# Kernel tuning notes

Hardware: AMD Instinct MI355X
Metric: run time of the kernel (lower is better)

Reference implementation:

```python
import jax, jax.numpy as jnp
import numpy as np

# RecursiveNN: leaves -> embedding lookup; internal node -> sum of two children.
# For a binary tree, the root value equals the sum of all leaf embeddings,
# so the batched faithful form is gather + reduce over the leaf axis.

VOCAB = 100000
DIM = 300
B = 4096   # number of trees (sentences)
L = 64     # leaves per tree


def setup_inputs() -> dict:
    key = jax.random.key(0)
    k1, k2 = jax.random.split(key)
    word_ids = jax.random.randint(k1, (B, L), 0, VOCAB, dtype=jnp.int64 if jax.config.jax_enable_x64 else jnp.int32)
    embedding = jax.random.normal(k2, (VOCAB, DIM), dtype=jnp.float32)
    return {"word_ids": word_ids, "embedding": embedding}


def reference(word_ids, embedding):
    # [B, L, D] gather of leaf embeddings, then child-sum reduction to the root: [B, D]
    leaf_emb = embedding[word_ids]
    return leaf_emb.sum(axis=1)
```

## Files before the change

### kernel.cpp

```cpp
#include <hip/hip_runtime.h>


#define NB 4096
#define NL 64
#define ND 300
#define ND4 75

__global__ __launch_bounds__(256, 4) void recnn_root_sum(
    const int* __restrict__ word_ids,
    const float4* __restrict__ emb4,
    float* __restrict__ out)
{
    __shared__ int ids[NL];
    __shared__ float partial[4][ND];

    const int b    = blockIdx.x;
    const int tid  = threadIdx.x;
    const int wave = tid >> 6;
    const int lane = tid & 63;

    if (tid < NL) ids[tid] = word_ids[b * NL + tid];
    __syncthreads();

    float4 acc0 = make_float4(0.f, 0.f, 0.f, 0.f);
    float4 acc1 = make_float4(0.f, 0.f, 0.f, 0.f);

    const int l0 = wave * 16;
    #pragma unroll
    for (int i = 0; i < 16; ++i) {
        const int row = ids[l0 + i];
        const float4* rp = emb4 + (size_t)row * ND4;
        float4 v0 = rp[lane];
        acc0.x += v0.x; acc0.y += v0.y; acc0.z += v0.z; acc0.w += v0.w;
        if (lane < ND4 - 64) {
            float4 v1 = rp[64 + lane];
            acc1.x += v1.x; acc1.y += v1.y; acc1.z += v1.z; acc1.w += v1.w;
        }
    }

    *reinterpret_cast<float4*>(&partial[wave][lane * 4]) = acc0;
    if (lane < ND4 - 64)
        *reinterpret_cast<float4*>(&partial[wave][256 + lane * 4]) = acc1;
    __syncthreads();

    for (int t = tid; t < ND; t += 256) {
        out[(size_t)b * ND + t] =
            partial[0][t] + partial[1][t] + partial[2][t] + partial[3][t];
    }
}

extern "C" void kernel_launch(void* const* d_in, const int* in_sizes, int n_in,
                              void* d_out, int out_size, void* d_ws, size_t ws_size,
                              hipStream_t stream) {
    const int*    word_ids = (const int*)d_in[0];
    const float4* emb4     = (const float4*)d_in[1];
    float*        out      = (float*)d_out;

    recnn_root_sum<<<NB, 256, 0, stream>>>(word_ids, emb4, out);
}
```

Baseline: 192.3 us.

## Assign one wave per tree and broadcast leaf ids via readlane

Each wave now reduces a whole tree instead of splitting a tree's leaves across four waves. This removes the shared-memory partial sums and both block barriers. Leaf ids are loaded one per lane and broadcast with readlane, and the 11-lane tail runs as a second loop that re-reads the ids. In exchange each wave issues a longer serial chain of 64 dependent-address loads with less parallelism per tree, and the tail loop runs with only 11 lanes active.

```diff
diff --git a/kernel.cpp b/kernel.cpp
--- a/kernel.cpp
+++ b/kernel.cpp
@@ -6,46 +6,39 @@
 #define ND 300
 #define ND4 75
 
-__global__ __launch_bounds__(256, 4) void recnn_root_sum(
+__global__ __launch_bounds__(256, 8) void recnn_root_sum(
     const int* __restrict__ word_ids,
     const float4* __restrict__ emb4,
-    float* __restrict__ out)
+    float4* __restrict__ out4)
 {
-    __shared__ int ids[NL];
-    __shared__ float partial[4][ND];
-
-    const int b    = blockIdx.x;
     const int tid  = threadIdx.x;
     const int wave = tid >> 6;
     const int lane = tid & 63;
+    const int tree = blockIdx.x * 4 + wave;
 
-    if (tid < NL) ids[tid] = word_ids[b * NL + tid];
-    __syncthreads();
+    const int myid = word_ids[tree * NL + lane];
 
     float4 acc0 = make_float4(0.f, 0.f, 0.f, 0.f);
-    float4 acc1 = make_float4(0.f, 0.f, 0.f, 0.f);
 
-    const int l0 = wave * 16;
-    #pragma unroll
-    for (int i = 0; i < 16; ++i) {
-        const int row = ids[l0 + i];
-        const float4* rp = emb4 + (size_t)row * ND4;
-        float4 v0 = rp[lane];
-        acc0.x += v0.x; acc0.y += v0.y; acc0.z += v0.z; acc0.w += v0.w;
-        if (lane < ND4 - 64) {
-            float4 v1 = rp[64 + lane];
-            acc1.x += v1.x; acc1.y += v1.y; acc1.z += v1.z; acc1.w += v1.w;
-        }
+    #pragma unroll 8
+    for (int i = 0; i < NL; ++i) {
+        const int row = __builtin_amdgcn_readlane(myid, i);
+        const float4 v = emb4[(size_t)row * ND4 + lane];
+        acc0.x += v.x; acc0.y += v.y; acc0.z += v.z; acc0.w += v.w;
     }
 
-    *reinterpret_cast<float4*>(&partial[wave][lane * 4]) = acc0;
-    if (lane < ND4 - 64)
-        *reinterpret_cast<float4*>(&partial[wave][256 + lane * 4]) = acc1;
-    __syncthreads();
+    float4* op = out4 + (size_t)tree * ND4;
+    op[lane] = acc0;
 
-    for (int t = tid; t < ND; t += 256) {
-        out[(size_t)b * ND + t] =
-            partial[0][t] + partial[1][t] + partial[2][t] + partial[3][t];
+    if (lane < ND4 - 64) {
+        float4 acc1 = make_float4(0.f, 0.f, 0.f, 0.f);
+        #pragma unroll 8
+        for (int i = 0; i < NL; ++i) {
+            const int row = __builtin_amdgcn_readlane(myid, i);
+            const float4 v = emb4[(size_t)row * ND4 + 64 + lane];
+            acc1.x += v.x; acc1.y += v.y; acc1.z += v.z; acc1.w += v.w;
+        }
+        op[64 + lane] = acc1;
     }
 }
 
@@ -54,7 +47,7 @@
                               hipStream_t stream) {
     const int*    word_ids = (const int*)d_in[0];
     const float4* emb4     = (const float4*)d_in[1];
-    float*        out      = (float*)d_out;
+    float4*       out4     = (float4*)d_out;
 
-    recnn_root_sum<<<NB, 256, 0, stream>>>(word_ids, emb4, out);
+    recnn_root_sum<<<NB / 4, 256, 0, stream>>>(word_ids, emb4, out4);
 }
```

Measured after the change: 196.7 us. +2.3%, slower.
